# Kernel optimization log

Measured on AMD Instinct MI355X. Metric: run time of the kernel, lower is better.

Reference implementation:

```python
import jax, jax.numpy as jnp
import numpy as np

COMMITMENT_FACTOR = 0.25
QUANTIZATION_FACTOR = 1.0
KL_FACTOR = 0.0  # default kl_loss_factor


def setup_inputs() -> dict:
    key = jax.random.key(0)
    k1, k2 = jax.random.split(key)
    B, S, D, K = 4096, 8, 512, 4096
    z = jax.random.normal(k1, (B, S, D), dtype=jnp.float32)
    # codebook initialized ~ U(-1/sqrt(D), 1/sqrt(D)) in the original; scale accordingly
    embeddings = jax.random.uniform(k2, (K, D), dtype=jnp.float32,
                                    minval=-1.0 / np.sqrt(D), maxval=1.0 / np.sqrt(D))
    return {"z": z, "embeddings": embeddings}


def reference(z, embeddings):
    sg = jax.lax.stop_gradient
    D = z.shape[-1]
    K = embeddings.shape[0]
    zf = z.reshape(-1, D)  # [N, D]
    # squared euclidean distances via expansion: ||z||^2 + ||e||^2 - 2 z e^T  -> [N, K]
    distances = ((zf ** 2).sum(-1, keepdims=True)
                 + (embeddings ** 2).sum(-1)
                 - 2.0 * zf @ embeddings.T)
    closest = jnp.argmin(distances, axis=-1)  # [N]
    quantized_indices = closest.reshape(z.shape[:-1])  # [B, S]
    # one-hot @ codebook == gather
    quantized = embeddings[closest].reshape(z.shape)  # [B, S, D]

    commitment_loss = jnp.mean((sg(quantized) - z) ** 2)
    embedding_loss = jnp.mean((quantized - sg(z)) ** 2)
    # KL(uniform || softmax(-d)), batchmean over rows
    log_p = jax.nn.log_softmax(-distances, axis=-1)
    kl_loss = jnp.mean(jnp.sum((1.0 / K) * (-jnp.log(jnp.float32(K)) - log_p), axis=-1))

    loss = (commitment_loss * COMMITMENT_FACTOR
            + embedding_loss * QUANTIZATION_FACTOR
            + kl_loss * KL_FACTOR)
    # straight-through estimator (non-gumbel path)
    quantized_st = z + sg(quantized - z)
    return loss, quantized_st, quantized_indices
```

## Files before the change

### kernel.cpp

```cpp
#include <hip/hip_runtime.h>
#include <cstdint>
#include <cmath>

#define N_ROWS 32768
#define DIM    512
#define KCODES 4096
#define SPLITS 2
#define CPS    (KCODES / SPLITS)
#define KCL    (CPS / 64)
#define TPS    (KCL * 4)
#define BM     128
#define TAU    2e-3f
#define CAP    1024
#define RQ     8

typedef _Float16 f16x8 __attribute__((ext_vector_type(8)));
typedef float    f32x4 __attribute__((ext_vector_type(4)));

#define OFF_NH  1048576
#define OFF_EN  (OFF_NH + KCODES)
#define OFF_R1  (OFF_EN + KCODES)
#define OFF_R2  (OFF_R1 + SPLITS * N_ROWS)
#define OFF_I1  (OFF_R2 + SPLITS * N_ROWS)
#define OFF_FI  (OFF_I1 + SPLITS * N_ROWS)
#define OFF_BI  (OFF_FI + N_ROWS)
#define OFF_BS  (OFF_BI + N_ROWS)
#define OFF_CT  (OFF_BS + 2048)
#define OFF_LR  (OFF_CT + 4)
#define OFF_LS  (OFF_LR + CAP)
#define OFF_SL  (OFF_LS + CAP)

__device__ __forceinline__ bool lexGT(float v1, int i1, float v2, int i2) {
  return (v1 > v2) || (v1 == v2 && i1 < i2);
}

__device__ __forceinline__ void gload16(const void* g, void* l) {
  __builtin_amdgcn_global_load_lds(
      (const __attribute__((address_space(1))) unsigned int*)g,
      (__attribute__((address_space(3))) unsigned int*)l, 16, 0, 0);
}

__device__ float np_sumsq_512(const float* __restrict__ a) {
#pragma clang fp contract(off)
  float B[4];
#pragma unroll
  for (int t = 0; t < 4; ++t) {
    const float* p = a + t * 128;
    float r[8];
    {
      float4 x0 = *(const float4*)p;
      float4 x1 = *(const float4*)(p + 4);
      r[0] = x0.x * x0.x; r[1] = x0.y * x0.y; r[2] = x0.z * x0.z; r[3] = x0.w * x0.w;
      r[4] = x1.x * x1.x; r[5] = x1.y * x1.y; r[6] = x1.z * x1.z; r[7] = x1.w * x1.w;
    }
    for (int i = 8; i < 128; i += 8) {
      float4 x0 = *(const float4*)(p + i);
      float4 x1 = *(const float4*)(p + i + 4);
      float f[8] = {x0.x, x0.y, x0.z, x0.w, x1.x, x1.y, x1.z, x1.w};
#pragma unroll
      for (int j = 0; j < 8; ++j) {
        float sq = f[j] * f[j];
        r[j] = r[j] + sq;
      }
    }
    B[t] = ((r[0] + r[1]) + (r[2] + r[3])) + ((r[4] + r[5]) + (r[6] + r[7]));
  }
  return (B[0] + B[1]) + (B[2] + B[3]);
}

__global__ __launch_bounds__(256) void vq_prep(const float* __restrict__ emb,
                                               f16x8* __restrict__ img,
                                               float* __restrict__ Enp,
                                               float* __restrict__ negHalf,
                                               int* __restrict__ counter) {
  int gid = blockIdx.x * 256 + threadIdx.x;
  if (gid == 0) counter[0] = 0;
  if (gid < KCODES) {
    float E = np_sumsq_512(emb + (size_t)gid * DIM);
    Enp[gid] = E;
    negHalf[gid] = -0.5f * E;
  }
  int T = gid >> 10, rem = gid & 1023;
  int fb = rem >> 6, lane = rem & 63;
  int kcg = T >> 2, dci = T & 3;
  int ks = fb >> 2, ct = fb & 3;
  int gh = lane >> 4, tl = lane & 15;
  int k = kcg * 64 + ct * 16 + tl;
  int d = dci * 128 + (ks * 4 + gh) * 8;
  const float* ep = emb + (size_t)k * DIM + d;
  float4 a = *(const float4*)ep;
  float4 b = *(const float4*)(ep + 4);
  float f[8] = {a.x, a.y, a.z, a.w, b.x, b.y, b.z, b.w};
  f16x8 h;
#pragma unroll
  for (int j = 0; j < 8; ++j) h[j] = (_Float16)f[j];
  img[gid] = h;
}

__global__ __launch_bounds__(256, 2) void vq_main(const float* __restrict__ z,
                                                  const f16x8* __restrict__ img,
                                                  const float* __restrict__ negHalf,
                                                  float* __restrict__ R1s,
                                                  float* __restrict__ R2s,
                                                  int* __restrict__ I1s) {
  __shared__ f16x8 EHs[2048];

  const int tid  = threadIdx.x;
  const int w    = tid >> 6;
  const int lane = tid & 63;
  const int tl   = lane & 15;
  const int gh   = lane >> 4;
  const int bid  = blockIdx.x;
  const int rb   = bid >> 1;
  const int sp   = bid & 1;
  const int m0   = rb * BM;

  f16x8 zh[2][16];
#pragma unroll
  for (int rt = 0; rt < 2; ++rt) {
    const float* zp = z + (size_t)(m0 + w * 32 + rt * 16 + tl) * DIM + gh * 8;
#pragma unroll
    for (int c = 0; c < 16; ++c) {
      float4 a = *(const float4*)(zp + c * 32);
      float4 b = *(const float4*)(zp + c * 32 + 4);
      float f[8] = {a.x, a.y, a.z, a.w, b.x, b.y, b.z, b.w};
      f16x8 h;
#pragma unroll
      for (int j = 0; j < 8; ++j) h[j] = (_Float16)f[j];
      zh[rt][c] = h;
    }
  }

  float R1[8], R2[8];
  int   I1u[8];
#pragma unroll
  for (int i = 0; i < 8; ++i) { R1[i] = -INFINITY; R2[i] = -INFINITY; I1u[i] = 0x7fffffff; }

  const f16x8* tbase = img + (size_t)sp * TPS * 1024;

  {
    const char* g = (const char*)tbase + w * 4096 + lane * 16;
    char* l = (char*)EHs + w * 4096;
#pragma unroll
    for (int i = 0; i < 4; ++i) gload16(g + i * 1024, l + i * 1024);
  }
  __syncthreads();

  for (int kcl = 0; kcl < KCL; ++kcl) {
    f32x4 acc[2][4];
#pragma unroll
    for (int ct = 0; ct < 4; ++ct) {
      float nh = negHalf[sp * CPS + kcl * 64 + ct * 16 + tl];
      acc[0][ct] = (f32x4){nh, nh, nh, nh};
      acc[1][ct] = (f32x4){nh, nh, nh, nh};
    }

#pragma unroll
    for (int dci = 0; dci < 4; ++dci) {
      const int t = kcl * 4 + dci;
      const int cur = t & 1;
      if (t + 1 < TPS) {
        const char* g = (const char*)(tbase + (size_t)(t + 1) * 1024) + w * 4096 + lane * 16;
        char* l = (char*)EHs + (cur ^ 1) * 16384 + w * 4096;
#pragma unroll
        for (int i = 0; i < 4; ++i) gload16(g + i * 1024, l + i * 1024);
      }
      const f16x8* B = EHs + cur * 1024;
#pragma unroll
      for (int ks = 0; ks < 4; ++ks) {
        {
          f16x8 bf0 = B[(ks * 4 + 0) * 64 + lane];
          f16x8 bf1 = B[(ks * 4 + 1) * 64 + lane];
          acc[0][0] = __builtin_amdgcn_mfma_f32_16x16x32_f16(zh[0][dci * 4 + ks], bf0, acc[0][0], 0, 0, 0);
          acc[1][0] = __builtin_amdgcn_mfma_f32_16x16x32_f16(zh[1][dci * 4 + ks], bf0, acc[1][0], 0, 0, 0);
          acc[0][1] = __builtin_amdgcn_mfma_f32_16x16x32_f16(zh[0][dci * 4 + ks], bf1, acc[0][1], 0, 0, 0);
          acc[1][1] = __builtin_amdgcn_mfma_f32_16x16x32_f16(zh[1][dci * 4 + ks], bf1, acc[1][1], 0, 0, 0);
        }
        {
          f16x8 bf2 = B[(ks * 4 + 2) * 64 + lane];
          f16x8 bf3 = B[(ks * 4 + 3) * 64 + lane];
          acc[0][2] = __builtin_amdgcn_mfma_f32_16x16x32_f16(zh[0][dci * 4 + ks], bf2, acc[0][2], 0, 0, 0);
          acc[1][2] = __builtin_amdgcn_mfma_f32_16x16x32_f16(zh[1][dci * 4 + ks], bf2, acc[1][2], 0, 0, 0);
          acc[0][3] = __builtin_amdgcn_mfma_f32_16x16x32_f16(zh[0][dci * 4 + ks], bf3, acc[0][3], 0, 0, 0);
          acc[1][3] = __builtin_amdgcn_mfma_f32_16x16x32_f16(zh[1][dci * 4 + ks], bf3, acc[1][3], 0, 0, 0);
        }
      }
      if (dci < 3) __syncthreads();
    }

#pragma unroll
    for (int ct = 0; ct < 4; ++ct) {
      const int cu = sp * CPS + kcl * 64 + ct * 16;
#pragma unroll
      for (int rt = 0; rt < 2; ++rt)
#pragma unroll
        for (int i = 0; i < 4; ++i) {
          int r8 = rt * 4 + i;
          float v = acc[rt][ct][i];
          float u = fminf(v, R1[r8]);
          R2[r8] = fmaxf(u, R2[r8]);
          bool gt = v > R1[r8];
          R1[r8] = fmaxf(v, R1[r8]);
          I1u[r8] = gt ? cu : I1u[r8];
        }
    }
    __syncthreads();
  }

  float R1f[8], R2f[8];
  int   I1f[8];
#pragma unroll
  for (int i = 0; i < 8; ++i) { R1f[i] = R1[i]; R2f[i] = R2[i]; I1f[i] = I1u[i] + tl; }

#pragma unroll
  for (int m = 1; m < 16; m <<= 1) {
#pragma unroll
    for (int i = 0; i < 8; ++i) {
      float o1 = __shfl_xor(R1f[i], m, 16);
      int   p1 = __shfl_xor(I1f[i], m, 16);
      float o2 = __shfl_xor(R2f[i], m, 16);
      R2f[i] = fmaxf(fmaxf(R2f[i], o2), fminf(R1f[i], o1));
      if (lexGT(o1, p1, R1f[i], I1f[i])) { R1f[i] = o1; I1f[i] = p1; }
    }
  }

  if (tl == 0) {
#pragma unroll
    for (int i = 0; i < 8; ++i) {
      int row = m0 + w * 32 + (i >> 2) * 16 + gh * 4 + (i & 3);
      R1s[(size_t)sp * N_ROWS + row] = R1f[i];
      R2s[(size_t)sp * N_ROWS + row] = R2f[i];
      I1s[(size_t)sp * N_ROWS + row] = I1f[i];
    }
  }
}

__global__ __launch_bounds__(256) void vq_merge(const float* __restrict__ z,
                                                const float* __restrict__ R1s,
                                                const float* __restrict__ R2s,
                                                const int* __restrict__ I1s,
                                                int* __restrict__ flagidx,
                                                int* __restrict__ bi,
                                                float* __restrict__ outIdx,
                                                int* __restrict__ counter,
                                                int* __restrict__ listRow,
                                                float* __restrict__ listS,
                                                unsigned long long* __restrict__ slots) {
  int row = blockIdx.x * 256 + threadIdx.x;
  float bR = -INFINITY, sec = -INFINITY;
  int bI = 0x7fffffff;
#pragma unroll
  for (int s = 0; s < SPLITS; ++s) {
    float r1 = R1s[(size_t)s * N_ROWS + row];
    float r2 = R2s[(size_t)s * N_ROWS + row];
    int   i1 = I1s[(size_t)s * N_ROWS + row];
    sec = fmaxf(fmaxf(sec, r2), fminf(bR, r1));
    if (lexGT(r1, i1, bR, bI)) { bR = r1; bI = i1; }
  }
  bi[row] = bI;
  outIdx[row] = (float)bI;
  int fi = 0;
  if (bR - sec < TAU) {
#pragma clang fp contract(off)
    int pos = atomicAdd(counter, 1);
    if (pos < CAP) {
      listRow[pos] = row;
      listS[pos]   = np_sumsq_512(z + (size_t)row * DIM);
      slots[pos]   = ~0ull;
      fi = pos + 1;
    }
  }
  flagidx[row] = fi;
}

__global__ __launch_bounds__(256) void vq_rescan(const float* __restrict__ z,
                                                 const float* __restrict__ emb,
                                                 const float* __restrict__ Enp,
                                                 const int* __restrict__ counter,
                                                 const int* __restrict__ listRow,
                                                 const float* __restrict__ listS,
                                                 unsigned long long* __restrict__ slots) {
  __shared__ unsigned long long sred[4][RQ];
  const int tid = threadIdx.x;
  const int ci  = blockIdx.x & 15;
  const int gi  = blockIdx.x >> 4;
  const int c   = ci * 256 + tid;
  const float* er = emb + (size_t)c * DIM;
  const float En = Enp[c];
  int n = counter[0];
  if (n > CAP) n = CAP;
  for (int qt = gi * RQ; qt < n; qt += 128 * RQ) {
#pragma clang fp contract(off)
    int q[RQ];
    const float* zr[RQ];
#pragma unroll
    for (int j = 0; j < RQ; ++j) {
      int qq = qt + j;
      q[j] = qq < n ? qq : n - 1;
      zr[j] = z + (size_t)listRow[q[j]] * DIM;
    }
    float a[RQ];
#pragma unroll
    for (int j = 0; j < RQ; ++j) a[j] = 0.f;
#pragma unroll 2
    for (int d0 = 0; d0 < DIM; d0 += 4) {
      float4 e = *(const float4*)(er + d0);
#pragma unroll
      for (int j = 0; j < RQ; ++j) {
        float4 x = *(const float4*)(zr[j] + d0);
        a[j] = fmaf(x.x, e.x, a[j]);
        a[j] = fmaf(x.y, e.y, a[j]);
        a[j] = fmaf(x.z, e.z, a[j]);
        a[j] = fmaf(x.w, e.w, a[j]);
      }
    }
#pragma unroll
    for (int j = 0; j < RQ; ++j) {
      float t = listS[q[j]] + En;
      float d = t - 2.0f * a[j];
      unsigned long long p =
          ((unsigned long long)__builtin_bit_cast(unsigned int, d) << 32) | (unsigned int)c;
#pragma unroll
      for (int m = 1; m < 64; m <<= 1) {
        unsigned long long o = __shfl_xor(p, m, 64);
        p = o < p ? o : p;
      }
      if ((tid & 63) == 0) sred[tid >> 6][j] = p;
    }
    __syncthreads();
    if (tid < RQ) {
      int j = tid;
      unsigned long long b = sred[0][j];
#pragma unroll
      for (int w2 = 1; w2 < 4; ++w2) b = sred[w2][j] < b ? sred[w2][j] : b;
      atomicMin(&slots[q[j]], b);
    }
    __syncthreads();
  }
}

__global__ __launch_bounds__(256) void vq_epi(const float* __restrict__ z,
                                              const float* __restrict__ emb,
                                              const int* __restrict__ bi,
                                              const int* __restrict__ flagidx,
                                              const unsigned long long* __restrict__ slots,
                                              float* __restrict__ out,
                                              float* __restrict__ outIdx,
                                              float* __restrict__ blockSums) {
  __shared__ float wred[4];
  int tid = threadIdx.x;
  int g = tid >> 4, tl = tid & 15;
  int row = blockIdx.x * 16 + g;
  int fi = flagidx[row];
  int code = bi[row];
  if (fi) {
    code = (int)(unsigned int)slots[fi - 1];
    if (tl == 0) outIdx[row] = (float)code;
  }
  const float* zr = z + (size_t)row * DIM;
  const float* er = emb + (size_t)code * DIM;
  float* oq = out + 1 + (size_t)row * DIM;
  float ls = 0.f;
#pragma unroll
  for (int j = 0; j < 8; ++j) {
    int d0 = (j * 16 + tl) * 4;
    float4 e = *(const float4*)(er + d0);
    float4 zz = *(const float4*)(zr + d0);
    float dx = e.x - zz.x, dy = e.y - zz.y, dz = e.z - zz.z, dw = e.w - zz.w;
    ls = fmaf(dx, dx, ls); ls = fmaf(dy, dy, ls);
    ls = fmaf(dz, dz, ls); ls = fmaf(dw, dw, ls);
    oq[d0 + 0] = e.x; oq[d0 + 1] = e.y; oq[d0 + 2] = e.z; oq[d0 + 3] = e.w;
  }
#pragma unroll
  for (int m = 1; m < 64; m <<= 1) ls += __shfl_xor(ls, m, 64);
  if ((tid & 63) == 0) wred[tid >> 6] = ls;
  __syncthreads();
  if (tid == 0) blockSums[blockIdx.x] = wred[0] + wred[1] + wred[2] + wred[3];
}

__global__ __launch_bounds__(256) void vq_final(const float* __restrict__ blockSums,
                                                float* __restrict__ out) {
  __shared__ float red[256];
  int t = threadIdx.x;
  float s = 0.f;
#pragma unroll
  for (int i = 0; i < 8; ++i) s += blockSums[t + i * 256];
  red[t] = s;
  __syncthreads();
  for (int k = 128; k > 0; k >>= 1) {
    if (t < k) red[t] += red[t + k];
    __syncthreads();
  }
  if (t == 0) out[0] = red[0] * (1.25f / 16777216.0f);
}

extern "C" void kernel_launch(void* const* d_in, const int* in_sizes, int n_in,
                              void* d_out, int out_size, void* d_ws, size_t ws_size,
                              hipStream_t stream) {
  const float* z   = (const float*)d_in[0];
  const float* emb = (const float*)d_in[1];
  float* out  = (float*)d_out;
  float* wsf  = (float*)d_ws;
  f16x8* img      = (f16x8*)d_ws;
  float* negHalf  = wsf + OFF_NH;
  float* Enp      = wsf + OFF_EN;
  float* R1s      = wsf + OFF_R1;
  float* R2s      = wsf + OFF_R2;
  int*   I1s      = (int*)(wsf + OFF_I1);
  int*   flagidx  = (int*)(wsf + OFF_FI);
  int*   bi       = (int*)(wsf + OFF_BI);
  float* bsums    = wsf + OFF_BS;
  int*   counter  = (int*)(wsf + OFF_CT);
  int*   listRow  = (int*)(wsf + OFF_LR);
  float* listS    = wsf + OFF_LS;
  unsigned long long* slots = (unsigned long long*)(wsf + OFF_SL);
  float* outIdx   = out + 1 + (size_t)N_ROWS * DIM;
  (void)in_sizes; (void)n_in; (void)out_size; (void)ws_size;

  vq_prep    <<<1024, 256, 0, stream>>>(emb, img, Enp, negHalf, counter);
  vq_main    <<<N_ROWS / BM * SPLITS, 256, 0, stream>>>(z, img, negHalf, R1s, R2s, I1s);
  vq_merge   <<<N_ROWS / 256, 256, 0, stream>>>(z, R1s, R2s, I1s, flagidx, bi, outIdx,
                                                counter, listRow, listS, slots);
  vq_rescan  <<<2048, 256, 0, stream>>>(z, emb, Enp, counter, listRow, listS, slots);
  vq_epi     <<<N_ROWS / 16, 256, 0, stream>>>(z, emb, bi, flagidx, slots, out, outIdx, bsums);
  vq_final   <<<1, 256, 0, stream>>>(bsums, out);
}
```

Baseline: 276.5 us.

## Compute quantization loss algebraically from argmin scores instead of rereading z

The per-row squared error is now formed as ||z||^2 - 2*best_score. The ||z||^2 term is computed in the main kernel from the fp16-converted z registers and reduced in the merge kernel. This lets the epilogue skip reading z a second time and only gather and write codebook rows. The trade-off is precision: the loss now depends on fp16-rounded z and the approximate MMA scores, and rows corrected by the rescan do not update the loss term.

```diff
diff --git a/kernel.cpp b/kernel.cpp
--- a/kernel.cpp
+++ b/kernel.cpp
@@ -29,6 +29,7 @@
 #define OFF_LR  (OFF_CT + 4)
 #define OFF_LS  (OFF_LR + CAP)
 #define OFF_SL  (OFF_LS + CAP)
+#define OFF_ZQ  (OFF_SL + 2 * CAP)
 
 __device__ __forceinline__ bool lexGT(float v1, int i1, float v2, int i2) {
   return (v1 > v2) || (v1 == v2 && i1 < i2);
@@ -102,7 +103,8 @@
                                                   const float* __restrict__ negHalf,
                                                   float* __restrict__ R1s,
                                                   float* __restrict__ R2s,
-                                                  int* __restrict__ I1s) {
+                                                  int* __restrict__ I1s,
+                                                  float* __restrict__ zsq) {
   __shared__ f16x8 EHs[2048];
 
   const int tid  = threadIdx.x;
@@ -128,6 +130,22 @@
 #pragma unroll
       for (int j = 0; j < 8; ++j) h[j] = (_Float16)f[j];
       zh[rt][c] = h;
+    }
+  }
+
+  if (sp == 0) {
+#pragma unroll
+    for (int rt = 0; rt < 2; ++rt) {
+      float s = 0.f;
+#pragma unroll
+      for (int c = 0; c < 16; ++c) {
+        f16x8 h = zh[rt][c];
+#pragma unroll
+        for (int j = 0; j < 8; ++j) { float v = (float)h[j]; s = fmaf(v, v, s); }
+      }
+      s += __shfl_xor(s, 16);
+      s += __shfl_xor(s, 32);
+      if (gh == 0) zsq[m0 + w * 32 + rt * 16 + tl] = s;
     }
   }
 
@@ -239,13 +257,16 @@
                                                 const float* __restrict__ R1s,
                                                 const float* __restrict__ R2s,
                                                 const int* __restrict__ I1s,
+                                                const float* __restrict__ zsq,
                                                 int* __restrict__ flagidx,
                                                 int* __restrict__ bi,
                                                 float* __restrict__ outIdx,
                                                 int* __restrict__ counter,
                                                 int* __restrict__ listRow,
                                                 float* __restrict__ listS,
-                                                unsigned long long* __restrict__ slots) {
+                                                unsigned long long* __restrict__ slots,
+                                                float* __restrict__ blockSums) {
+  __shared__ float wred[4];
   int row = blockIdx.x * 256 + threadIdx.x;
   float bR = -INFINITY, sec = -INFINITY;
   int bI = 0x7fffffff;
@@ -271,6 +292,14 @@
     }
   }
   flagidx[row] = fi;
+
+  float lp = zsq[row] - 2.0f * bR;
+#pragma unroll
+  for (int m = 1; m < 64; m <<= 1) lp += __shfl_xor(lp, m);
+  if ((threadIdx.x & 63) == 0) wred[threadIdx.x >> 6] = lp;
+  __syncthreads();
+  if (threadIdx.x == 0)
+    blockSums[blockIdx.x] = wred[0] + wred[1] + wred[2] + wred[3];
 }
 
 __global__ __launch_bounds__(256) void vq_rescan(const float* __restrict__ z,
@@ -339,15 +368,12 @@
   }
 }
 
-__global__ __launch_bounds__(256) void vq_epi(const float* __restrict__ z,
-                                              const float* __restrict__ emb,
+__global__ __launch_bounds__(256) void vq_epi(const float* __restrict__ emb,
                                               const int* __restrict__ bi,
                                               const int* __restrict__ flagidx,
                                               const unsigned long long* __restrict__ slots,
                                               float* __restrict__ out,
-                                              float* __restrict__ outIdx,
-                                              float* __restrict__ blockSums) {
-  __shared__ float wred[4];
+                                              float* __restrict__ outIdx) {
   int tid = threadIdx.x;
   int g = tid >> 4, tl = tid & 15;
   int row = blockIdx.x * 16 + g;
@@ -357,37 +383,23 @@
     code = (int)(unsigned int)slots[fi - 1];
     if (tl == 0) outIdx[row] = (float)code;
   }
-  const float* zr = z + (size_t)row * DIM;
   const float* er = emb + (size_t)code * DIM;
   float* oq = out + 1 + (size_t)row * DIM;
-  float ls = 0.f;
 #pragma unroll
   for (int j = 0; j < 8; ++j) {
     int d0 = (j * 16 + tl) * 4;
     float4 e = *(const float4*)(er + d0);
-    float4 zz = *(const float4*)(zr + d0);
-    float dx = e.x - zz.x, dy = e.y - zz.y, dz = e.z - zz.z, dw = e.w - zz.w;
-    ls = fmaf(dx, dx, ls); ls = fmaf(dy, dy, ls);
-    ls = fmaf(dz, dz, ls); ls = fmaf(dw, dw, ls);
     oq[d0 + 0] = e.x; oq[d0 + 1] = e.y; oq[d0 + 2] = e.z; oq[d0 + 3] = e.w;
   }
-#pragma unroll
-  for (int m = 1; m < 64; m <<= 1) ls += __shfl_xor(ls, m, 64);
-  if ((tid & 63) == 0) wred[tid >> 6] = ls;
+}
+
+__global__ __launch_bounds__(128) void vq_final(const float* __restrict__ blockSums,
+                                                float* __restrict__ out) {
+  __shared__ float red[128];
+  int t = threadIdx.x;
+  red[t] = blockSums[t];
   __syncthreads();
-  if (tid == 0) blockSums[blockIdx.x] = wred[0] + wred[1] + wred[2] + wred[3];
-}
-
-__global__ __launch_bounds__(256) void vq_final(const float* __restrict__ blockSums,
-                                                float* __restrict__ out) {
-  __shared__ float red[256];
-  int t = threadIdx.x;
-  float s = 0.f;
-#pragma unroll
-  for (int i = 0; i < 8; ++i) s += blockSums[t + i * 256];
-  red[t] = s;
-  __syncthreads();
-  for (int k = 128; k > 0; k >>= 1) {
+  for (int k = 64; k > 0; k >>= 1) {
     if (t < k) red[t] += red[t + k];
     __syncthreads();
   }
@@ -414,14 +426,15 @@
   int*   listRow  = (int*)(wsf + OFF_LR);
   float* listS    = wsf + OFF_LS;
   unsigned long long* slots = (unsigned long long*)(wsf + OFF_SL);
+  float* zsq      = wsf + OFF_ZQ;
   float* outIdx   = out + 1 + (size_t)N_ROWS * DIM;
   (void)in_sizes; (void)n_in; (void)out_size; (void)ws_size;
 
   vq_prep    <<<1024, 256, 0, stream>>>(emb, img, Enp, negHalf, counter);
-  vq_main    <<<N_ROWS / BM * SPLITS, 256, 0, stream>>>(z, img, negHalf, R1s, R2s, I1s);
-  vq_merge   <<<N_ROWS / 256, 256, 0, stream>>>(z, R1s, R2s, I1s, flagidx, bi, outIdx,
-                                                counter, listRow, listS, slots);
+  vq_main    <<<N_ROWS / BM * SPLITS, 256, 0, stream>>>(z, img, negHalf, R1s, R2s, I1s, zsq);
+  vq_merge   <<<N_ROWS / 256, 256, 0, stream>>>(z, R1s, R2s, I1s, zsq, flagidx, bi, outIdx,
+                                                counter, listRow, listS, slots, bsums);
   vq_rescan  <<<2048, 256, 0, stream>>>(z, emb, Enp, counter, listRow, listS, slots);
-  vq_epi     <<<N_ROWS / 16, 256, 0, stream>>>(z, emb, bi, flagidx, slots, out, outIdx, bsums);
-  vq_final   <<<1, 256, 0, stream>>>(bsums, out);
-}
+  vq_epi     <<<N_ROWS / 16, 256, 0, stream>>>(emb, bi, flagidx, slots, out, outIdx);
+  vq_final   <<<1, 128, 0, stream>>>(bsums, out);
+}
```

After: 287.6 us. +4.0%, slower.
